# Kernel tuning notes

Hardware: AMD Instinct MI355X
Metric: run time of the kernel (lower is better)

The kernel has to match this reference:

```python
import jax, jax.numpy as jnp
import numpy as np

B, IN, CTX, OUT = 4096, 256, 64, 128
N, K, J = 128, 4, 64            # n_neurons, n_branches, branch_size (both layers)
NG = N * K                      # gates per layer = 512
WS = IN * NG                    # gating weight count per layer (gating always sees original x)
TP = 2 * (WS + NG)              # total hypernetwork output params = 263168
S = 0.05


def setup_inputs() -> dict:
    key = jax.random.key(0)
    ks = jax.random.split(key, 20)
    r = lambda i, shape: jax.random.normal(ks[i], shape, dtype=jnp.float32) * S
    return {
        "x": jax.random.normal(ks[0], (B, IN), dtype=jnp.float32),
        "context": jax.random.normal(ks[1], (CTX,), dtype=jnp.float32),
        # layer 0 (in=256): per-neuron per-branch linear + soma
        "Wb0": r(2, (N, K, J, IN)), "bb0": r(3, (N, K, J)),
        "Ws0": r(4, (N, K * J)),    "bs0": r(5, (N,)),
        # layer 1 (in=128)
        "Wb1": r(6, (N, K, J, N)),  "bb1": r(7, (N, K, J)),
        "Ws1": r(8, (N, K * J)),    "bs1": r(9, (N,)),
        # output layer
        "Wout": r(10, (OUT, N)), "bout": r(11, (OUT,)),
        # hypernetwork: ctx -> 32 -> 64 -> TP
        "h1w": r(12, (32, CTX)), "h1b": r(13, (32,)),
        "h2w": r(14, (64, 32)),  "h2b": r(15, (64,)),
        "h3w": r(16, (TP, 64)),  "h3b": r(17, (TP,)),
    }


def _dann_layer(cur, x, gw_slice, Wb, bb, Ws, bs):
    # gating weights derived from hypernetwork output vector (shared across batch)
    Wg = gw_slice[:WS].reshape(NG, IN)
    bg = gw_slice[WS:WS + NG]
    gates = jax.nn.sigmoid(x @ Wg.T + bg).reshape(-1, N, K, 1)      # [B,N,K,1]
    h = jax.nn.relu(jnp.einsum('bi,nkji->bnkj', cur, Wb) + bb) * gates
    return jnp.einsum('bnkj,nkj->bn', h, Ws.reshape(N, K, J)) + bs  # [B,N]


def reference(x, context, Wb0, bb0, Ws0, bs0, Wb1, bb1, Ws1, bs1,
              Wout, bout, h1w, h1b, h2w, h2b, h3w, h3b):
    # hypernetwork (dropout inactive at inference); single context -> one weight vector
    hv = jax.nn.relu(context @ h1w.T + h1b)
    hv = jax.nn.relu(hv @ h2w.T + h2b)
    gw = hv @ h3w.T + h3b                                           # [TP]
    per = WS + NG
    cur = _dann_layer(x,   x, gw[:per],        Wb0, bb0, Ws0, bs0)
    cur = _dann_layer(cur, x, gw[per:2 * per], Wb1, bb1, Ws1, bs1)
    return cur @ Wout.T + bout
```

## Files before the change

### kernel.cpp

```cpp
#include <hip/hip_runtime.h>

#define BB   4096
#define IN_  256
#define NN   128
#define KK   4
#define JJ   64
#define NG   512
#define WS_  131072
#define PER  131584
#define TP   263168
#define OUTD 128

typedef __attribute__((ext_vector_type(8))) short short8;
typedef __attribute__((ext_vector_type(4))) float f32x4;

#define VW(N) asm volatile("s_waitcnt vmcnt(" #N ")" ::: "memory")

__device__ __forceinline__ unsigned short f2bf(float f){
  unsigned u = __float_as_uint(f);
  return (unsigned short)((u + 0x7fffu + ((u >> 16) & 1u)) >> 16);
}

__device__ __forceinline__ void gload16(const void* g, void* l){
  __builtin_amdgcn_global_load_lds((const __attribute__((address_space(1))) void*)g,
                                   (__attribute__((address_space(3))) void*)l, 16, 0, 0);
}

#define XE  (4096u*256u)
#define W0E (XE + 8388608u)
#define W1E (W0E + 4194304u)

__global__ void k_convert(const float* __restrict__ x,
                          const float* __restrict__ w0,
                          const float* __restrict__ w1,
                          unsigned short* __restrict__ xb,
                          unsigned short* __restrict__ w0b,
                          unsigned short* __restrict__ w1b){
  size_t i = ((size_t)blockIdx.x*256 + threadIdx.x)*4;
  if (i >= W1E) return;
  const float* s; unsigned short* d; size_t off;
  if (i < XE)       { s = x;  d = xb;  off = i; }
  else if (i < W0E) { s = w0; d = w0b; off = i - XE; }
  else              { s = w1; d = w1b; off = i - W0E; }
  float4 v = *(const float4*)(s + off);
  ushort4 o;
  o.x = f2bf(v.x); o.y = f2bf(v.y); o.z = f2bf(v.z); o.w = f2bf(v.w);
  *(ushort4*)(d + off) = o;
}

__global__ void k_hyper(const float* __restrict__ ctx,
                        const float* __restrict__ h1w, const float* __restrict__ h1b,
                        const float* __restrict__ h2w, const float* __restrict__ h2b,
                        float* __restrict__ hv2){
  __shared__ float s1[32];
  int t = threadIdx.x;
  if (t < 32){
    float a = h1b[t];
    #pragma unroll 8
    for (int i = 0; i < 64; ++i) a += ctx[i]*h1w[t*64+i];
    s1[t] = fmaxf(a, 0.f);
  }
  __syncthreads();
  float a = h2b[t];
  #pragma unroll 8
  for (int i = 0; i < 32; ++i) a += s1[i]*h2w[t*32+i];
  hv2[t] = fmaxf(a, 0.f);
}

__global__ void k_gw(const float* __restrict__ hv2,
                     const float* __restrict__ h3w, const float* __restrict__ h3b,
                     unsigned short* __restrict__ Wg_bf, float* __restrict__ bg){
  int t = threadIdx.x;
  int r = blockIdx.x*64 + (t >> 2);
  int q = t & 3;
  const float4* row = (const float4*)(h3w + (size_t)r*64);
  float a = 0.f;
  #pragma unroll
  for (int i = 0; i < 4; ++i){
    float4 v = row[q*4 + i];
    float4 h = *(const float4*)(hv2 + q*16 + i*4);
    a += v.x*h.x + v.y*h.y + v.z*h.z + v.w*h.w;
  }
  a += __shfl_xor(a, 1);
  a += __shfl_xor(a, 2);
  if (q == 0){
    a += h3b[r];
    if (r < WS_)          Wg_bf[r] = f2bf(a);
    else if (r < PER)     bg[r - WS_] = a;
    else if (r < PER+WS_) Wg_bf[WS_ + (r - PER)] = f2bf(a);
    else                  bg[512 + (r - (PER+WS_))] = a;
  }
}

__global__ __launch_bounds__(512, 1)
void k_gates(const unsigned short* __restrict__ Wg_bf,
             const unsigned short* __restrict__ x_bf,
             const float* __restrict__ bg,
             float* __restrict__ GT){
  __shared__ __align__(16) unsigned short As[128*64];
  __shared__ __align__(16) unsigned short Bs[256*64];
  const int tid  = threadIdx.x;
  const int lane = tid & 63;
  const int wid  = tid >> 6;
  const int wm = wid >> 2, wn = wid & 3;
  const int lrow = lane & 15, lk = lane >> 4;
  const int m0 = blockIdx.x*128;
  const int b0 = blockIdx.y*256;

  f32x4 zero = {0.f,0.f,0.f,0.f};
  f32x4 acc[4][4];
  #pragma unroll
  for (int i=0;i<4;++i)
    #pragma unroll
    for (int j=0;j<4;++j) acc[i][j] = zero;

  for (int kt = 0; kt < 256/64; ++kt){
    __syncthreads();
    #pragma unroll
    for (int i = 0; i < 2; ++i){
      int c = tid + i*512;
      int row = c >> 3, k8 = c & 7;
      uint4 v = *(const uint4*)(Wg_bf + (size_t)(m0+row)*256 + kt*64 + k8*8);
      int idx = (row*64 + k8*8) ^ ((row & 7) << 3);
      *(uint4*)(&As[idx]) = v;
    }
    #pragma unroll
    for (int i = 0; i < 4; ++i){
      int c = tid + i*512;
      int row = c >> 3, k8 = c & 7;
      uint4 v = *(const uint4*)(x_bf + (size_t)(b0+row)*256 + kt*64 + k8*8);
      int idx = (row*64 + k8*8) ^ ((row & 7) << 3);
      *(uint4*)(&Bs[idx]) = v;
    }
    __syncthreads();
    #pragma unroll
    for (int kk = 0; kk < 2; ++kk){
      short8 a[4], b[4];
      #pragma unroll
      for (int fm = 0; fm < 4; ++fm){
        int m = wm*64 + fm*16 + lrow;
        int idx = (m*64 + kk*32 + lk*8) ^ ((m & 7) << 3);
        a[fm] = *(const short8*)(&As[idx]);
      }
      #pragma unroll
      for (int fn = 0; fn < 4; ++fn){
        int r = wn*64 + fn*16 + lrow;
        int idx = (r*64 + kk*32 + lk*8) ^ ((r & 7) << 3);
        b[fn] = *(const short8*)(&Bs[idx]);
      }
      #pragma unroll
      for (int fm = 0; fm < 4; ++fm)
        #pragma unroll
        for (int fn = 0; fn < 4; ++fn)
          acc[fm][fn] = __builtin_amdgcn_mfma_f32_16x16x32_bf16(a[fm], b[fn], acc[fm][fn], 0, 0, 0);
    }
  }
  #pragma unroll
  for (int fm = 0; fm < 4; ++fm){
    float4 bgv = *(const float4*)(bg + m0 + wm*64 + fm*16 + lk*4);
    float bga[4] = {bgv.x, bgv.y, bgv.z, bgv.w};
    #pragma unroll
    for (int reg = 0; reg < 4; ++reg){
      int m = m0 + wm*64 + fm*16 + lk*4 + reg;
      #pragma unroll
      for (int fn = 0; fn < 4; ++fn){
        int b = b0 + wn*64 + fn*16 + lrow;
        float z = acc[fm][fn][reg] + bga[reg];
        GT[(size_t)m*4096 + b] = 1.f/(1.f + __expf(-z));
      }
    }
  }
}

template<int KIN, int LAYER>
__global__ __launch_bounds__(512, 1)
void k_layer(const unsigned short* __restrict__ Abf,
             const unsigned short* __restrict__ Wbf,
             const float* __restrict__ bb,
             const float* __restrict__ Ws,
             const float* __restrict__ GT,
             float* __restrict__ partg){
  constexpr int NT     = KIN/64;
  constexpr int SC     = (LAYER==0) ? 128 : 256;
  constexpr int WN     = (LAYER==0) ? 2 : 4;
  constexpr int WMN    = 8/WN;
  constexpr int BTR    = WMN*64;
  constexpr int NBT    = 16;
  constexpr int ABUFSZ = BTR*64;
  constexpr int WBOFF  = 2*ABUFSZ;
  constexpr int AI     = BTR/64;
  constexpr int WI     = SC/64;
  __shared__ __align__(16) unsigned short lds[WBOFF + SC*64*NT];

  const int tid  = threadIdx.x;
  const int lane = tid & 63;
  const int wid  = tid >> 6;
  const int wn   = wid % WN, wm = wid / WN;
  const int lrow = lane & 15, lk = lane >> 4;

  const int id      = blockIdx.x;
  const int n       = id >> 1;
  const int sub     = id & 1;
  const int kgrp    = (LAYER==0) ? sub*2 + wn : wn;
  const int abase   = (LAYER==0) ? 0 : sub*2048;
  const int colbase = n*256 + ((LAYER==0) ? sub*128 : 0);

  f32x4 zero = {0.f,0.f,0.f,0.f};
  f32x4 acc[4][4];
  #pragma unroll
  for (int i=0;i<4;++i)
    #pragma unroll
    for (int jj=0;jj<4;++jj) acc[i][jj] = zero;

  auto STAGE_A = [&](int buf, int bt, int kt){
    #pragma unroll
    for (int i = 0; i < AI; ++i){
      int c = i*512 + tid;
      int r = c >> 3, kc = c & 7;
      const unsigned short* s = Abf + (size_t)(abase + bt*BTR + r)*KIN + kt*64 + ((kc ^ (r&7))<<3);
      gload16(s, &lds[buf*ABUFSZ + (i*512 + wid*64)*8]);
    }
  };

  #pragma unroll
  for (int kt = 0; kt < NT; ++kt)
    #pragma unroll
    for (int i = 0; i < WI; ++i){
      int c = i*512 + tid;
      int r = c >> 3, kc = c & 7;
      const unsigned short* s = Wbf + (size_t)(colbase + r)*KIN + kt*64 + ((kc ^ (r&7))<<3);
      gload16(s, &lds[WBOFF + kt*SC*64 + (i*512 + wid*64)*8]);
    }
  STAGE_A(0, 0, 0);
  asm volatile("" ::: "memory");

  float bbv[4], wsv[4];
  #pragma unroll
  for (int fn = 0; fn < 4; ++fn){
    int cloc = ((LAYER==0) ? sub*128 : 0) + wn*64 + fn*16 + lrow;
    bbv[fn] = bb[n*256 + cloc];
    wsv[fn] = Ws[n*256 + cloc];
  }
  const float* gtrow = GT + (size_t)(LAYER*512 + n*4 + kgrp)*4096 + abase;
  float* prow = partg + (size_t)kgrp*524288 + (size_t)n*4096 + abase;

  int abuf = 0;
  #pragma unroll 1
  for (int bt = 0; bt < NBT; ++bt){
    float4 gv[4];
    #pragma unroll
    for (int kt = 0; kt < NT; ++kt){
      const int  ph  = bt*NT + kt;
      const bool epi = (kt == NT-1);

      if (ph == 0)      VW(0);
      else if (kt <= 1) VW(4);
      else              VW(0);
      __builtin_amdgcn_s_barrier();

      if (ph + 1 < NBT*NT){
        int bt2 = epi ? bt+1 : bt;
        int kt2 = epi ? 0    : kt+1;
        STAGE_A(abuf ^ 1, bt2, kt2);
      }
      asm volatile("" ::: "memory");

      if (kt == 0){
        #pragma unroll
        for (int fm = 0; fm < 4; ++fm)
          gv[fm] = *(const float4*)(gtrow + bt*BTR + wm*64 + fm*16 + lk*4);
        asm volatile("" ::: "memory");
      }

      #pragma unroll
      for (int kk = 0; kk < 2; ++kk){
        short8 a[4], b[4];
        #pragma unroll
        for (int fm = 0; fm < 4; ++fm){
          int m = wm*64 + fm*16 + lrow;
          int idx = abuf*ABUFSZ + ((m*64 + kk*32 + lk*8) ^ ((m & 7) << 3));
          a[fm] = *(const short8*)(&lds[idx]);
        }
        #pragma unroll
        for (int fn = 0; fn < 4; ++fn){
          int r = wn*64 + fn*16 + lrow;
          int idx = WBOFF + kt*SC*64 + ((r*64 + kk*32 + lk*8) ^ ((r & 7) << 3));
          b[fn] = *(const short8*)(&lds[idx]);
        }
        #pragma unroll
        for (int fm = 0; fm < 4; ++fm)
          #pragma unroll
          for (int fn = 0; fn < 4; ++fn)
            acc[fm][fn] = __builtin_amdgcn_mfma_f32_16x16x32_bf16(a[fm], b[fn], acc[fm][fn], 0, 0, 0);
      }

      if (epi){
        #pragma unroll
        for (int fm = 0; fm < 4; ++fm){
          float gr[4] = {gv[fm].x, gv[fm].y, gv[fm].z, gv[fm].w};
          float sums[4];
          #pragma unroll
          for (int reg = 0; reg < 4; ++reg){
            float s = 0.f;
            #pragma unroll
            for (int fn = 0; fn < 4; ++fn)
              s += fmaxf(acc[fm][fn][reg] + bbv[fn], 0.f) * wsv[fn];
            s *= gr[reg];
            s += __shfl_xor(s, 1);
            s += __shfl_xor(s, 2);
            s += __shfl_xor(s, 4);
            s += __shfl_xor(s, 8);
            sums[reg] = s;
          }
          if (lrow == 0){
            float4 o; o.x = sums[0]; o.y = sums[1]; o.z = sums[2]; o.w = sums[3];
            *(float4*)(prow + bt*BTR + wm*64 + fm*16 + lk*4) = o;
          }
        }
        #pragma unroll
        for (int i2 = 0; i2 < 4; ++i2)
          #pragma unroll
          for (int j2 = 0; j2 < 4; ++j2) acc[i2][j2] = zero;
      }
      abuf ^= 1;
    }
  }
}

template<int OUT_BF>
__global__ void k_mid(const float* __restrict__ partg, const float* __restrict__ bsv,
                      unsigned short* __restrict__ obf, float* __restrict__ of32){
  const int n = blockIdx.x;
  const int t = threadIdx.x;
  const float* p = partg + (size_t)n*4096 + t*16;
  const float bsn = bsv[n];
  #pragma unroll
  for (int i = 0; i < 4; ++i){
    float4 s0 = *(const float4*)(p + i*4);
    float4 s1 = *(const float4*)(p + 524288 + i*4);
    float4 s2 = *(const float4*)(p + 2*524288 + i*4);
    float4 s3 = *(const float4*)(p + 3*524288 + i*4);
    float v0 = ((s0.x + s1.x) + s2.x) + s3.x + bsn;
    float v1 = ((s0.y + s1.y) + s2.y) + s3.y + bsn;
    float v2 = ((s0.z + s1.z) + s2.z) + s3.z + bsn;
    float v3 = ((s0.w + s1.w) + s2.w) + s3.w + bsn;
    size_t b = (size_t)t*16 + i*4;
    if (OUT_BF){
      obf[(b+0)*128 + n] = f2bf(v0);
      obf[(b+1)*128 + n] = f2bf(v1);
      obf[(b+2)*128 + n] = f2bf(v2);
      obf[(b+3)*128 + n] = f2bf(v3);
    } else {
      of32[(b+0)*128 + n] = v0;
      of32[(b+1)*128 + n] = v1;
      of32[(b+2)*128 + n] = v2;
      of32[(b+3)*128 + n] = v3;
    }
  }
}

__global__ void k_final(const float* __restrict__ out1, const float* __restrict__ Wout,
                        const float* __restrict__ bout, float* __restrict__ out){
  int t = blockIdx.x*256 + threadIdx.x;
  int b = t >> 7, o = t & 127;
  const float4* cr = (const float4*)(out1 + (size_t)b*128);
  const float4* wr = (const float4*)(Wout + (size_t)o*128);
  float a = 0.f;
  #pragma unroll
  for (int i = 0; i < 32; ++i){
    float4 c = cr[i], w = wr[i];
    a += c.x*w.x + c.y*w.y + c.z*w.z + c.w*w.w;
  }
  out[t] = a + bout[o];
}

extern "C" void kernel_launch(void* const* d_in, const int* in_sizes, int n_in,
                              void* d_out, int out_size, void* d_ws, size_t ws_size,
                              hipStream_t stream){
  const float* x    = (const float*)d_in[0];
  const float* ctx  = (const float*)d_in[1];
  const float* Wb0  = (const float*)d_in[2];
  const float* bb0  = (const float*)d_in[3];
  const float* Ws0  = (const float*)d_in[4];
  const float* bs0  = (const float*)d_in[5];
  const float* Wb1  = (const float*)d_in[6];
  const float* bb1  = (const float*)d_in[7];
  const float* Ws1  = (const float*)d_in[8];
  const float* bs1  = (const float*)d_in[9];
  const float* Wout = (const float*)d_in[10];
  const float* bout = (const float*)d_in[11];
  const float* h1w  = (const float*)d_in[12];
  const float* h1b  = (const float*)d_in[13];
  const float* h2w  = (const float*)d_in[14];
  const float* h2b  = (const float*)d_in[15];
  const float* h3w  = (const float*)d_in[16];
  const float* h3b  = (const float*)d_in[17];
  float* out = (float*)d_out;

  char* ws = (char*)d_ws;
  size_t o = 0;
  unsigned short* x_bf  = (unsigned short*)(ws + o); o += (size_t)4096*256*2;
  unsigned short* W0b   = (unsigned short*)(ws + o); o += (size_t)8388608*2;
  unsigned short* W1b   = (unsigned short*)(ws + o); o += (size_t)4194304*2;
  unsigned short* Wg_bf = (unsigned short*)(ws + o); o += (size_t)1024*256*2;
  float* bg   = (float*)(ws + o); o += 1024*4;
  float* hv2  = (float*)(ws + o); o += 256;
  float* GT   = (float*)(ws + o); o += (size_t)1024*4096*4;
  unsigned short* cur_bf = (unsigned short*)(ws + o); o += (size_t)4096*128*2;
  float* out1 = (float*)(ws + o); o += (size_t)4096*128*4;
  float* partg0 = (float*)(ws + o); o += (size_t)4*128*4096*4;
  float* partg1 = (float*)W0b;

  k_convert<<<13312, 256, 0, stream>>>(x, Wb0, Wb1, x_bf, W0b, W1b);
  k_hyper<<<1, 64, 0, stream>>>(ctx, h1w, h1b, h2w, h2b, hv2);
  k_gw<<<4112, 256, 0, stream>>>(hv2, h3w, h3b, Wg_bf, bg);
  k_gates<<<dim3(8, 16), 512, 0, stream>>>(Wg_bf, x_bf, bg, GT);
  k_layer<256, 0><<<256, 512, 0, stream>>>(x_bf, W0b, bb0, Ws0, GT, partg0);
  k_mid<1><<<128, 256, 0, stream>>>(partg0, bs0, cur_bf, nullptr);
  k_layer<128, 1><<<256, 512, 0, stream>>>(cur_bf, W1b, bb1, Ws1, GT, partg1);
  k_mid<0><<<128, 256, 0, stream>>>(partg1, bs1, nullptr, out1);
  k_final<<<2048, 256, 0, stream>>>(out1, Wout, bout, out);
}
```

Baseline: 226.6 us.

## Keep branch weights in registers and stage activations in wider K chunks

Each wave now loads its slice of the bf16 branch weights straight into registers once, instead of staging them in LDS and re-reading them every phase. Only activation tiles pass through LDS, staged 128 K-columns per phase with double buffering, which halves the number of barriers and phases. The 16-lane row reduction in the epilogue now uses DPP row ops instead of shfl_xor. The cost is heavy register use (up to 128 VGPRs of weights in layer 0), which risks spills or lower scheduling freedom, plus a larger LDS footprint for the activation buffers.

New measurement: 238.9 us. +5.4%, slower.

```diff
diff --git a/kernel.cpp b/kernel.cpp
--- a/kernel.cpp
+++ b/kernel.cpp
@@ -24,6 +24,14 @@
 __device__ __forceinline__ void gload16(const void* g, void* l){
   __builtin_amdgcn_global_load_lds((const __attribute__((address_space(1))) void*)g,
                                    (__attribute__((address_space(3))) void*)l, 16, 0, 0);
+}
+
+__device__ __forceinline__ float rowred16(float s){
+  s += __int_as_float(__builtin_amdgcn_update_dpp(0, __float_as_int(s), 0xB1,  0xF, 0xF, true));
+  s += __int_as_float(__builtin_amdgcn_update_dpp(0, __float_as_int(s), 0x4E,  0xF, 0xF, true));
+  s += __int_as_float(__builtin_amdgcn_update_dpp(0, __float_as_int(s), 0x124, 0xF, 0xF, true));
+  s += __int_as_float(__builtin_amdgcn_update_dpp(0, __float_as_int(s), 0x128, 0xF, 0xF, true));
+  return s;
 }
 
 #define XE  (4096u*256u)
@@ -180,17 +188,14 @@
              const float* __restrict__ Ws,
              const float* __restrict__ GT,
              float* __restrict__ partg){
-  constexpr int NT     = KIN/64;
-  constexpr int SC     = (LAYER==0) ? 128 : 256;
-  constexpr int WN     = (LAYER==0) ? 2 : 4;
-  constexpr int WMN    = 8/WN;
-  constexpr int BTR    = WMN*64;
-  constexpr int NBT    = 16;
-  constexpr int ABUFSZ = BTR*64;
-  constexpr int WBOFF  = 2*ABUFSZ;
-  constexpr int AI     = BTR/64;
-  constexpr int WI     = SC/64;
-  __shared__ __align__(16) unsigned short lds[WBOFF + SC*64*NT];
+  constexpr int BTR   = (LAYER==0) ? 256 : 128;
+  constexpr int WN    = (LAYER==0) ? 2 : 4;
+  constexpr int KSL   = KIN/32;
+  constexpr int PPB   = KIN/128;
+  constexpr int NBT   = 16;
+  constexpr int NPH   = NBT*PPB;
+  constexpr int ABUF  = BTR*128;
+  __shared__ __align__(16) unsigned short lds[2*ABUF];
 
   const int tid  = threadIdx.x;
   const int lane = tid & 63;
@@ -212,25 +217,29 @@
     #pragma unroll
     for (int jj=0;jj<4;++jj) acc[i][jj] = zero;
 
+  short8 breg[KSL][4];
+  {
+    const unsigned short* wrow = Wbf + (size_t)(colbase + wn*64 + lrow)*KIN + lk*8;
+    #pragma unroll
+    for (int ks = 0; ks < KSL; ++ks)
+      #pragma unroll
+      for (int fn = 0; fn < 4; ++fn)
+        breg[ks][fn] = *(const short8*)(wrow + (size_t)fn*16*KIN + ks*32);
+  }
+
   auto STAGE_A = [&](int buf, int bt, int kt){
     #pragma unroll
-    for (int i = 0; i < AI; ++i){
-      int c = i*512 + tid;
-      int r = c >> 3, kc = c & 7;
-      const unsigned short* s = Abf + (size_t)(abase + bt*BTR + r)*KIN + kt*64 + ((kc ^ (r&7))<<3);
-      gload16(s, &lds[buf*ABUFSZ + (i*512 + wid*64)*8]);
-    }
+    for (int ktl = 0; ktl < 2; ++ktl)
+      #pragma unroll
+      for (int ii = 0; ii < BTR/64; ++ii){
+        int c = ii*512 + tid;
+        int r = c >> 3, kc = c & 7;
+        const unsigned short* s = Abf + (size_t)(abase + bt*BTR + r)*KIN
+                                  + kt*128 + ktl*64 + ((kc ^ (r&7))<<3);
+        gload16(s, &lds[buf*ABUF + ktl*BTR*64 + (ii*512 + wid*64)*8]);
+      }
   };
 
-  #pragma unroll
-  for (int kt = 0; kt < NT; ++kt)
-    #pragma unroll
-    for (int i = 0; i < WI; ++i){
-      int c = i*512 + tid;
-      int r = c >> 3, kc = c & 7;
-      const unsigned short* s = Wbf + (size_t)(colbase + r)*KIN + kt*64 + ((kc ^ (r&7))<<3);
-      gload16(s, &lds[WBOFF + kt*SC*64 + (i*512 + wid*64)*8]);
-    }
   STAGE_A(0, 0, 0);
   asm volatile("" ::: "memory");
 
@@ -247,25 +256,25 @@
   int abuf = 0;
   #pragma unroll 1
   for (int bt = 0; bt < NBT; ++bt){
-    float4 gv[4];
-    #pragma unroll
-    for (int kt = 0; kt < NT; ++kt){
-      const int  ph  = bt*NT + kt;
-      const bool epi = (kt == NT-1);
+    #pragma unroll
+    for (int kt = 0; kt < PPB; ++kt){
+      const int  ph  = bt*PPB + kt;
+      const bool epi = (kt == PPB-1);
 
       if (ph == 0)      VW(0);
-      else if (kt <= 1) VW(4);
+      else if (kt == 0) VW(8);
       else              VW(0);
       __builtin_amdgcn_s_barrier();
 
-      if (ph + 1 < NBT*NT){
-        int bt2 = epi ? bt+1 : bt;
-        int kt2 = epi ? 0    : kt+1;
+      if (ph + 1 < NPH){
+        int bt2 = bt, kt2 = kt + 1;
+        if (kt2 == PPB){ kt2 = 0; bt2 = bt + 1; }
         STAGE_A(abuf ^ 1, bt2, kt2);
       }
       asm volatile("" ::: "memory");
 
-      if (kt == 0){
+      float4 gv[4];
+      if (epi){
         #pragma unroll
         for (int fm = 0; fm < 4; ++fm)
           gv[fm] = *(const float4*)(gtrow + bt*BTR + wm*64 + fm*16 + lk*4);
@@ -273,25 +282,21 @@
       }
 
       #pragma unroll
-      for (int kk = 0; kk < 2; ++kk){
-        short8 a[4], b[4];
+      for (int kk = 0; kk < 4; ++kk){
+        short8 a[4];
         #pragma unroll
         for (int fm = 0; fm < 4; ++fm){
           int m = wm*64 + fm*16 + lrow;
-          int idx = abuf*ABUFSZ + ((m*64 + kk*32 + lk*8) ^ ((m & 7) << 3));
+          int idx = abuf*ABUF + (kk>>1)*BTR*64
+                    + ((m*64 + (kk&1)*32 + lk*8) ^ ((m & 7) << 3));
           a[fm] = *(const short8*)(&lds[idx]);
-        }
-        #pragma unroll
-        for (int fn = 0; fn < 4; ++fn){
-          int r = wn*64 + fn*16 + lrow;
-          int idx = WBOFF + kt*SC*64 + ((r*64 + kk*32 + lk*8) ^ ((r & 7) << 3));
-          b[fn] = *(const short8*)(&lds[idx]);
         }
         #pragma unroll
         for (int fm = 0; fm < 4; ++fm)
           #pragma unroll
           for (int fn = 0; fn < 4; ++fn)
-            acc[fm][fn] = __builtin_amdgcn_mfma_f32_16x16x32_bf16(a[fm], b[fn], acc[fm][fn], 0, 0, 0);
+            acc[fm][fn] = __builtin_amdgcn_mfma_f32_16x16x32_bf16(
+                a[fm], breg[kt*4 + kk][fn], acc[fm][fn], 0, 0, 0);
       }
 
       if (epi){
@@ -305,12 +310,7 @@
             #pragma unroll
             for (int fn = 0; fn < 4; ++fn)
               s += fmaxf(acc[fm][fn][reg] + bbv[fn], 0.f) * wsv[fn];
-            s *= gr[reg];
-            s += __shfl_xor(s, 1);
-            s += __shfl_xor(s, 2);
-            s += __shfl_xor(s, 4);
-            s += __shfl_xor(s, 8);
-            sums[reg] = s;
+            sums[reg] = rowred16(s * gr[reg]);
           }
           if (lrow == 0){
             float4 o; o.x = sums[0]; o.y = sums[1]; o.z = sums[2]; o.w = sums[3];
```

## Fuse weight bf16 conversion into layer kernels and merge hypernetwork kernels

Applied to the files above, without the earlier changes.

The separate pass that converted the branch weights Wb0/Wb1 to bf16 in global memory is removed. Each layer block now loads its fp32 weight slice directly, converts it in registers and writes it swizzled into LDS. The two hypernetwork kernels are merged so each block recomputes the small first MLP stages before its h3 rows, and the partial-sum shuffles become DPP row reductions with precomputed LDS offsets. This drops a full write and re-read of the converted weights and one launch, at the cost of redundant tiny MLP work per block and doubled fp32 weight read bytes in the layer prologue.

Result: faster. 214.1 us (-5.5%).

```diff
diff --git a/kernel.cpp b/kernel.cpp
--- a/kernel.cpp
+++ b/kernel.cpp
@@ -3,13 +3,10 @@
 #define BB   4096
 #define IN_  256
 #define NN   128
-#define KK   4
-#define JJ   64
 #define NG   512
 #define WS_  131072
 #define PER  131584
 #define TP   263168
-#define OUTD 128
 
 typedef __attribute__((ext_vector_type(8))) short short8;
 typedef __attribute__((ext_vector_type(4))) float f32x4;
@@ -26,34 +23,31 @@
                                    (__attribute__((address_space(3))) void*)l, 16, 0, 0);
 }
 
-#define XE  (4096u*256u)
-#define W0E (XE + 8388608u)
-#define W1E (W0E + 4194304u)
-
-__global__ void k_convert(const float* __restrict__ x,
-                          const float* __restrict__ w0,
-                          const float* __restrict__ w1,
-                          unsigned short* __restrict__ xb,
-                          unsigned short* __restrict__ w0b,
-                          unsigned short* __restrict__ w1b){
+__device__ __forceinline__ float rowred16(float s){
+  s += __int_as_float(__builtin_amdgcn_update_dpp(0, __float_as_int(s), 0xB1,  0xF, 0xF, true));
+  s += __int_as_float(__builtin_amdgcn_update_dpp(0, __float_as_int(s), 0x4E,  0xF, 0xF, true));
+  s += __int_as_float(__builtin_amdgcn_update_dpp(0, __float_as_int(s), 0x124, 0xF, 0xF, true));
+  s += __int_as_float(__builtin_amdgcn_update_dpp(0, __float_as_int(s), 0x128, 0xF, 0xF, true));
+  return s;
+}
+
+__global__ void k_convert(const float* __restrict__ x, unsigned short* __restrict__ xb){
   size_t i = ((size_t)blockIdx.x*256 + threadIdx.x)*4;
-  if (i >= W1E) return;
-  const float* s; unsigned short* d; size_t off;
-  if (i < XE)       { s = x;  d = xb;  off = i; }
-  else if (i < W0E) { s = w0; d = w0b; off = i - XE; }
-  else              { s = w1; d = w1b; off = i - W0E; }
-  float4 v = *(const float4*)(s + off);
+  float4 v = *(const float4*)(x + i);
   ushort4 o;
   o.x = f2bf(v.x); o.y = f2bf(v.y); o.z = f2bf(v.z); o.w = f2bf(v.w);
-  *(ushort4*)(d + off) = o;
-}
-
-__global__ void k_hyper(const float* __restrict__ ctx,
-                        const float* __restrict__ h1w, const float* __restrict__ h1b,
-                        const float* __restrict__ h2w, const float* __restrict__ h2b,
-                        float* __restrict__ hv2){
+  *(ushort4*)(xb + i) = o;
+}
+
+__global__ __launch_bounds__(512)
+void k_gw(const float* __restrict__ ctx,
+          const float* __restrict__ h1w, const float* __restrict__ h1b,
+          const float* __restrict__ h2w, const float* __restrict__ h2b,
+          const float* __restrict__ h3w, const float* __restrict__ h3b,
+          unsigned short* __restrict__ Wg_bf, float* __restrict__ bg){
   __shared__ float s1[32];
-  int t = threadIdx.x;
+  __shared__ float hv2[64];
+  const int t = threadIdx.x;
   if (t < 32){
     float a = h1b[t];
     #pragma unroll 8
@@ -61,28 +55,24 @@
     s1[t] = fmaxf(a, 0.f);
   }
   __syncthreads();
-  float a = h2b[t];
-  #pragma unroll 8
-  for (int i = 0; i < 32; ++i) a += s1[i]*h2w[t*32+i];
-  hv2[t] = fmaxf(a, 0.f);
-}
-
-__global__ void k_gw(const float* __restrict__ hv2,
-                     const float* __restrict__ h3w, const float* __restrict__ h3b,
-                     unsigned short* __restrict__ Wg_bf, float* __restrict__ bg){
-  int t = threadIdx.x;
-  int r = blockIdx.x*64 + (t >> 2);
-  int q = t & 3;
+  if (t < 64){
+    float a = h2b[t];
+    #pragma unroll 8
+    for (int i = 0; i < 32; ++i) a += s1[i]*h2w[t*32+i];
+    hv2[t] = fmaxf(a, 0.f);
+  }
+  __syncthreads();
+
+  const int r = blockIdx.x*64 + (t >> 3);
+  const int q = t & 7;
   const float4* row = (const float4*)(h3w + (size_t)r*64);
-  float a = 0.f;
-  #pragma unroll
-  for (int i = 0; i < 4; ++i){
-    float4 v = row[q*4 + i];
-    float4 h = *(const float4*)(hv2 + q*16 + i*4);
-    a += v.x*h.x + v.y*h.y + v.z*h.z + v.w*h.w;
-  }
+  float4 v0 = row[q*2], v1 = row[q*2+1];
+  float4 h0 = *(const float4*)(hv2 + q*8), h1 = *(const float4*)(hv2 + q*8 + 4);
+  float a = v0.x*h0.x + v0.y*h0.y + v0.z*h0.z + v0.w*h0.w
+          + v1.x*h1.x + v1.y*h1.y + v1.z*h1.z + v1.w*h1.w;
   a += __shfl_xor(a, 1);
   a += __shfl_xor(a, 2);
+  a += __shfl_xor(a, 4);
   if (q == 0){
     a += h3b[r];
     if (r < WS_)          Wg_bf[r] = f2bf(a);
@@ -175,7 +165,7 @@
 template<int KIN, int LAYER>
 __global__ __launch_bounds__(512, 1)
 void k_layer(const unsigned short* __restrict__ Abf,
-             const unsigned short* __restrict__ Wbf,
+             const float* __restrict__ Wf32,
              const float* __restrict__ bb,
              const float* __restrict__ Ws,
              const float* __restrict__ GT,
@@ -183,14 +173,15 @@
   constexpr int NT     = KIN/64;
   constexpr int SC     = (LAYER==0) ? 128 : 256;
   constexpr int WN     = (LAYER==0) ? 2 : 4;
-  constexpr int WMN    = 8/WN;
-  constexpr int BTR    = WMN*64;
+  constexpr int BTR    = (LAYER==0) ? 256 : 128;
   constexpr int NBT    = 16;
-  constexpr int ABUFSZ = BTR*64;
-  constexpr int WBOFF  = 2*ABUFSZ;
   constexpr int AI     = BTR/64;
-  constexpr int WI     = SC/64;
-  __shared__ __align__(16) unsigned short lds[WBOFF + SC*64*NT];
+  constexpr int ABUFS  = BTR*64;
+  constexpr unsigned ABYTES = ABUFS*2;
+  constexpr int WBOFFS = 2*ABUFS;
+  constexpr unsigned WBYTES = WBOFFS*2;
+  constexpr unsigned KTB = SC*64*2;
+  __shared__ __align__(16) unsigned short lds[WBOFFS + SC*64*NT];
 
   const int tid  = threadIdx.x;
   const int lane = tid & 63;
@@ -218,21 +209,40 @@
       int c = i*512 + tid;
       int r = c >> 3, kc = c & 7;
       const unsigned short* s = Abf + (size_t)(abase + bt*BTR + r)*KIN + kt*64 + ((kc ^ (r&7))<<3);
-      gload16(s, &lds[buf*ABUFSZ + (i*512 + wid*64)*8]);
+      gload16(s, &lds[buf*ABUFS + (i*512 + wid*64)*8]);
     }
   };
 
-  #pragma unroll
-  for (int kt = 0; kt < NT; ++kt)
-    #pragma unroll
-    for (int i = 0; i < WI; ++i){
-      int c = i*512 + tid;
-      int r = c >> 3, kc = c & 7;
-      const unsigned short* s = Wbf + (size_t)(colbase + r)*KIN + kt*64 + ((kc ^ (r&7))<<3);
-      gload16(s, &lds[WBOFF + kt*SC*64 + (i*512 + wid*64)*8]);
-    }
   STAGE_A(0, 0, 0);
   asm volatile("" ::: "memory");
+  {
+    constexpr int CHPR = KIN/8;
+    #pragma unroll
+    for (int half = 0; half < 2; ++half){
+      float4 va[4], vb[4];
+      #pragma unroll
+      for (int j = 0; j < 4; ++j){
+        int c = (half*4 + j)*512 + tid;
+        int r = c / CHPR, q = c % CHPR;
+        const float4* s = (const float4*)(Wf32 + (size_t)(colbase + r)*KIN + q*8);
+        va[j] = s[0]; vb[j] = s[1];
+      }
+      #pragma unroll
+      for (int j = 0; j < 4; ++j){
+        int c = (half*4 + j)*512 + tid;
+        int r = c / CHPR, q = c % CHPR;
+        int kt = q >> 3, k8 = q & 7;
+        short8 p;
+        p[0] = (short)f2bf(va[j].x); p[1] = (short)f2bf(va[j].y);
+        p[2] = (short)f2bf(va[j].z); p[3] = (short)f2bf(va[j].w);
+        p[4] = (short)f2bf(vb[j].x); p[5] = (short)f2bf(vb[j].y);
+        p[6] = (short)f2bf(vb[j].z); p[7] = (short)f2bf(vb[j].w);
+        int dst = WBOFFS + kt*SC*64 + ((r*64 + k8*8) ^ ((r&7)<<3));
+        *(short8*)(&lds[dst]) = p;
+      }
+    }
+  }
+  asm volatile("s_waitcnt lgkmcnt(0)" ::: "memory");
 
   float bbv[4], wsv[4];
   #pragma unroll
@@ -244,7 +254,20 @@
   const float* gtrow = GT + (size_t)(LAYER*512 + n*4 + kgrp)*4096 + abase;
   float* prow = partg + (size_t)kgrp*524288 + (size_t)n*4096 + abase;
 
-  int abuf = 0;
+  unsigned aoff[4], boff[4];
+  #pragma unroll
+  for (int fm = 0; fm < 4; ++fm){
+    int m = wm*64 + fm*16 + lrow;
+    aoff[fm] = 2u*((unsigned)((m*64 + lk*8) ^ ((m & 7) << 3)));
+  }
+  #pragma unroll
+  for (int fn = 0; fn < 4; ++fn){
+    int r = wn*64 + fn*16 + lrow;
+    boff[fn] = 2u*((unsigned)((r*64 + lk*8) ^ ((r & 7) << 3)));
+  }
+  const char* ldsc = (const char*)lds;
+  unsigned abufB = 0;
+
   #pragma unroll 1
   for (int bt = 0; bt < NBT; ++bt){
     float4 gv[4];
@@ -259,9 +282,9 @@
       __builtin_amdgcn_s_barrier();
 
       if (ph + 1 < NBT*NT){
-        int bt2 = epi ? bt+1 : bt;
-        int kt2 = epi ? 0    : kt+1;
-        STAGE_A(abuf ^ 1, bt2, kt2);
+        int bt2 = bt, kt2 = kt + 1;
+        if (kt2 == NT){ kt2 = 0; bt2 = bt + 1; }
+        STAGE_A(abufB ? 0 : 1, bt2, kt2);
       }
       asm volatile("" ::: "memory");
 
@@ -276,17 +299,11 @@
       for (int kk = 0; kk < 2; ++kk){
         short8 a[4], b[4];
         #pragma unroll
-        for (int fm = 0; fm < 4; ++fm){
-          int m = wm*64 + fm*16 + lrow;
-          int idx = abuf*ABUFSZ + ((m*64 + kk*32 + lk*8) ^ ((m & 7) << 3));
-          a[fm] = *(const short8*)(&lds[idx]);
-        }
-        #pragma unroll
-        for (int fn = 0; fn < 4; ++fn){
-          int r = wn*64 + fn*16 + lrow;
-          int idx = WBOFF + kt*SC*64 + ((r*64 + kk*32 + lk*8) ^ ((r & 7) << 3));
-          b[fn] = *(const short8*)(&lds[idx]);
-        }
+        for (int fm = 0; fm < 4; ++fm)
+          a[fm] = *(const short8*)(ldsc + (abufB + (aoff[fm] ^ (unsigned)(kk*64))));
+        #pragma unroll
+        for (int fn = 0; fn < 4; ++fn)
+          b[fn] = *(const short8*)(ldsc + WBYTES + kt*KTB + (boff[fn] ^ (unsigned)(kk*64)));
         #pragma unroll
         for (int fm = 0; fm < 4; ++fm)
           #pragma unroll
@@ -305,12 +322,7 @@
             #pragma unroll
             for (int fn = 0; fn < 4; ++fn)
               s += fmaxf(acc[fm][fn][reg] + bbv[fn], 0.f) * wsv[fn];
-            s *= gr[reg];
-            s += __shfl_xor(s, 1);
-            s += __shfl_xor(s, 2);
-            s += __shfl_xor(s, 4);
-            s += __shfl_xor(s, 8);
-            sums[reg] = s;
+            sums[reg] = rowred16(s * gr[reg]);
           }
           if (lrow == 0){
             float4 o; o.x = sums[0]; o.y = sums[1]; o.z = sums[2]; o.w = sums[3];
@@ -322,7 +334,7 @@
           #pragma unroll
           for (int j2 = 0; j2 < 4; ++j2) acc[i2][j2] = zero;
       }
-      abuf ^= 1;
+      abufB ^= ABYTES;
     }
   }
 }
@@ -400,24 +412,20 @@
   char* ws = (char*)d_ws;
   size_t o = 0;
   unsigned short* x_bf  = (unsigned short*)(ws + o); o += (size_t)4096*256*2;
-  unsigned short* W0b   = (unsigned short*)(ws + o); o += (size_t)8388608*2;
-  unsigned short* W1b   = (unsigned short*)(ws + o); o += (size_t)4194304*2;
   unsigned short* Wg_bf = (unsigned short*)(ws + o); o += (size_t)1024*256*2;
-  float* bg   = (float*)(ws + o); o += 1024*4;
-  float* hv2  = (float*)(ws + o); o += 256;
-  float* GT   = (float*)(ws + o); o += (size_t)1024*4096*4;
+  float* bg     = (float*)(ws + o); o += 1024*4;
+  float* GT     = (float*)(ws + o); o += (size_t)1024*4096*4;
   unsigned short* cur_bf = (unsigned short*)(ws + o); o += (size_t)4096*128*2;
-  float* out1 = (float*)(ws + o); o += (size_t)4096*128*4;
+  float* out1   = (float*)(ws + o); o += (size_t)4096*128*4;
   float* partg0 = (float*)(ws + o); o += (size_t)4*128*4096*4;
-  float* partg1 = (float*)W0b;
-
-  k_convert<<<13312, 256, 0, stream>>>(x, Wb0, Wb1, x_bf, W0b, W1b);
-  k_hyper<<<1, 64, 0, stream>>>(ctx, h1w, h1b, h2w, h2b, hv2);
-  k_gw<<<4112, 256, 0, stream>>>(hv2, h3w, h3b, Wg_bf, bg);
+  float* partg1 = (float*)(ws + o); o += (size_t)4*128*4096*4;
+
+  k_convert<<<1024, 256, 0, stream>>>(x, x_bf);
+  k_gw<<<4112, 512, 0, stream>>>(ctx, h1w, h1b, h2w, h2b, h3w, h3b, Wg_bf, bg);
   k_gates<<<dim3(8, 16), 512, 0, stream>>>(Wg_bf, x_bf, bg, GT);
-  k_layer<256, 0><<<256, 512, 0, stream>>>(x_bf, W0b, bb0, Ws0, GT, partg0);
+  k_layer<256, 0><<<256, 512, 0, stream>>>(x_bf, Wb0, bb0, Ws0, GT, partg0);
   k_mid<1><<<128, 256, 0, stream>>>(partg0, bs0, cur_bf, nullptr);
-  k_layer<128, 1><<<256, 512, 0, stream>>>(cur_bf, W1b, bb1, Ws1, GT, partg1);
+  k_layer<128, 1><<<256, 512, 0, stream>>>(cur_bf, Wb1, bb1, Ws1, GT, partg1);
   k_mid<0><<<128, 256, 0, stream>>>(partg1, bs1, nullptr, out1);
   k_final<<<2048, 256, 0, stream>>>(out1, Wout, bout, out);
 }
```
